# Kernel optimization log

Hardware: AMD Instinct MI355X
Metric: run time of the kernel (lower is better)

## Reference

```python
import jax, jax.numpy as jnp
import numpy as np

NUM_EMBEDDINGS = 1024
EMBEDDING_DIM = 64
COMMITMENT_COST = 0.25


def setup_inputs() -> dict:
    key = jax.random.key(0)
    k1, k2 = jax.random.split(key)
    inputs = jax.random.normal(k1, (64, 32, 32, EMBEDDING_DIM), dtype=jnp.float32)
    # matches nn.Embedding weight init: uniform(-1/K, 1/K)
    codebook = jax.random.uniform(
        k2, (NUM_EMBEDDINGS, EMBEDDING_DIM), dtype=jnp.float32,
        minval=-1.0 / NUM_EMBEDDINGS, maxval=1.0 / NUM_EMBEDDINGS)
    return {"inputs": inputs, "codebook": codebook}


def reference(inputs, codebook):
    input_shape = inputs.shape
    flat = inputs.reshape(-1, EMBEDDING_DIM)  # [N, D]
    distances = (jnp.sum(flat * flat, axis=1, keepdims=True)
                 + jnp.sum(codebook * codebook, axis=1)
                 - 2.0 * jnp.matmul(flat, codebook.T))
    encoding_indices = jnp.argmin(distances, axis=1)  # [N]
    quantized = codebook[encoding_indices].reshape(input_shape)
    codebook_loss = jnp.mean((jax.lax.stop_gradient(quantized) - inputs) ** 2)
    commitment_loss = jnp.mean((jax.lax.stop_gradient(inputs) - quantized) ** 2)
    vq_loss = codebook_loss + COMMITMENT_COST * commitment_loss
    # straight-through estimator
    quantized_st = inputs + jax.lax.stop_gradient(quantized - inputs)
    return quantized_st, vq_loss
```

## Files before the change

### kernel.cpp

```cpp
#include <hip/hip_runtime.h>

typedef __attribute__((ext_vector_type(8))) short short8;
typedef __attribute__((ext_vector_type(4))) float f32x4;
typedef __attribute__((ext_vector_type(4))) unsigned short u16x4;

#define NVEC 65536
#define DDIM 64
#define KCODES 1024
#define NELEM 4194304
#define CHUNK_C 128
#define VPB 128

__device__ inline unsigned short f2bf(float f) {
  unsigned u = __builtin_bit_cast(unsigned, f);
  return (unsigned short)((u + 0x7FFFu + ((u >> 16) & 1u)) >> 16);
}
__device__ inline float bf2f(unsigned short b) {
  unsigned u = ((unsigned)b) << 16;
  return __builtin_bit_cast(float, u);
}

__global__ __launch_bounds__(256) void vq_prep(const float* __restrict__ cb,
                                               unsigned short* __restrict__ cb_bf,
                                               float* __restrict__ en,
                                               float* __restrict__ out) {
  __shared__ float en_l[64];
  const int tid = threadIdx.x;
  if (tid < 64) en_l[tid] = 0.f;
  __syncthreads();
  const int base = blockIdx.x * 1024;
#pragma unroll
  for (int i = 0; i < 4; ++i) {
    int f = base + i * 256 + tid;
    float4 v = ((const float4*)cb)[f];
    unsigned short b0 = f2bf(v.x), b1 = f2bf(v.y), b2 = f2bf(v.z), b3 = f2bf(v.w);
    u16x4 pk = {b0, b1, b2, b3};
    *(u16x4*)(cb_bf + (size_t)f * 4) = pk;
    float e0 = bf2f(b0), e1 = bf2f(b1), e2 = bf2f(b2), e3 = bf2f(b3);
    atomicAdd(&en_l[(f >> 4) - blockIdx.x * 64], e0 * e0 + e1 * e1 + e2 * e2 + e3 * e3);
  }
  __syncthreads();
  if (tid < 64) en[blockIdx.x * 64 + tid] = en_l[tid];
  if (blockIdx.x == 0 && tid == 0) out[NELEM] = 0.f;
}

__global__ __launch_bounds__(256, 2) void vq_main(
    const float* __restrict__ x, const float* __restrict__ cb,
    const unsigned short* __restrict__ cb_bf, const float* __restrict__ en,
    float* __restrict__ out) {
  __shared__ alignas(16) unsigned short xs[8192];
  __shared__ alignas(16) unsigned short es[8192];
  __shared__ float en_s[CHUNK_C];
  __shared__ float xn[VPB];
  __shared__ float sbest[VPB];
  __shared__ int sidx[VPB];
  __shared__ float wsum[4];

  const int tid = threadIdx.x;
  const int wid = tid >> 6;
  const int L = tid & 63;
  const int q = L >> 4;
  const int c16 = L & 15;
  const int vblk = blockIdx.x * VPB;

  if (tid < VPB) xn[tid] = 0.f;
  __syncthreads();

#pragma unroll
  for (int i = 0; i < 4; ++i) {
    int f = i * 256 + tid;
    int fl = f & 63, fh = (f >> 6) & 1, fm = (f >> 7) & 1, fw = f >> 8;
    int v = fw * 32 + fm * 16 + (fl & 15);
    int d = fh * 32 + (fl >> 4) * 8;
    const float4* xp = (const float4*)(x + (size_t)(vblk + v) * DDIM + d);
    float4 u0 = xp[0], u1 = xp[1];
    unsigned short b0 = f2bf(u0.x), b1 = f2bf(u0.y), b2 = f2bf(u0.z), b3 = f2bf(u0.w);
    unsigned short b4 = f2bf(u1.x), b5 = f2bf(u1.y), b6 = f2bf(u1.z), b7 = f2bf(u1.w);
    float s0 = bf2f(b0), s1 = bf2f(b1), s2 = bf2f(b2), s3 = bf2f(b3);
    float s4 = bf2f(b4), s5 = bf2f(b5), s6 = bf2f(b6), s7 = bf2f(b7);
    atomicAdd(&xn[v], (s0 * s0 + s1 * s1 + s2 * s2 + s3 * s3) +
                          (s4 * s4 + s5 * s5 + s6 * s6 + s7 * s7));
    u16x4 p0 = {b0, b1, b2, b3}, p1 = {b4, b5, b6, b7};
    *(u16x4*)(xs + (size_t)f * 8) = p0;
    *(u16x4*)(xs + (size_t)f * 8 + 4) = p1;
  }
  __syncthreads();

  short8 a[2][2];
#pragma unroll
  for (int m = 0; m < 2; ++m)
#pragma unroll
    for (int h = 0; h < 2; ++h)
      a[m][h] = *(const short8*)(xs + (((wid * 4 + m * 2 + h) * 64 + L) * 8));

  float best[2][4];
  int bidx[2][4];
#pragma unroll
  for (int m = 0; m < 2; ++m)
#pragma unroll
    for (int r = 0; r < 4; ++r) {
      best[m][r] = 3.0e38f;
      bidx[m][r] = 0;
    }

  for (int c0 = 0; c0 < KCODES; c0 += CHUNK_C) {
    __syncthreads();
#pragma unroll
    for (int i = 0; i < 4; ++i) {
      int f = i * 256 + tid;
      int fl = f & 63, fh = (f >> 6) & 1, fnt = f >> 7;
      int code = c0 + fnt * 16 + (fl & 15);
      int d = fh * 32 + (fl >> 4) * 8;
      short8 v = *(const short8*)(cb_bf + (size_t)code * DDIM + d);
      *(short8*)(es + (size_t)f * 8) = v;
    }
    if (tid < CHUNK_C) en_s[tid] = en[c0 + tid];
    __syncthreads();

#pragma unroll
    for (int nt = 0; nt < 8; ++nt) {
      short8 b0 = *(const short8*)(es + ((nt * 2 + 0) * 64 + L) * 8);
      short8 b1 = *(const short8*)(es + ((nt * 2 + 1) * 64 + L) * 8);
      float env = en_s[nt * 16 + c16];
      int kidx = c0 + nt * 16 + c16;
#pragma unroll
      for (int m = 0; m < 2; ++m) {
        f32x4 z = {0.f, 0.f, 0.f, 0.f};
        f32x4 acc = __builtin_amdgcn_mfma_f32_16x16x32_bf16(a[m][0], b0, z, 0, 0, 0);
        acc = __builtin_amdgcn_mfma_f32_16x16x32_bf16(a[m][1], b1, acc, 0, 0, 0);
#pragma unroll
        for (int r = 0; r < 4; ++r) {
          float s = fmaf(-2.f, acc[r], env);
          if (s < best[m][r]) {
            best[m][r] = s;
            bidx[m][r] = kidx;
          }
        }
      }
    }
  }

#pragma unroll
  for (int m = 0; m < 2; ++m)
#pragma unroll
    for (int r = 0; r < 4; ++r) {
      float s = best[m][r];
      int id = bidx[m][r];
#pragma unroll
      for (int off = 1; off < 16; off <<= 1) {
        float s2 = __shfl_xor(s, off, 64);
        int i2 = __shfl_xor(id, off, 64);
        if (s2 < s || (s2 == s && i2 < id)) {
          s = s2;
          id = i2;
        }
      }
      if (c16 == 0) {
        int v = wid * 32 + m * 16 + q * 4 + r;
        sbest[v] = s;
        sidx[v] = id;
      }
    }
  __syncthreads();

#pragma unroll
  for (int i = 0; i < 8; ++i) {
    int f = i * 256 + tid;
    int v = f >> 4, d4 = f & 15;
    int id = sidx[v];
    float4 ev = ((const float4*)cb)[(size_t)id * 16 + d4];
    ((float4*)out)[(size_t)vblk * 16 + f] = ev;
  }

  float p = (tid < VPB) ? (sbest[tid] + xn[tid]) : 0.f;
#pragma unroll
  for (int off = 32; off >= 1; off >>= 1) p += __shfl_down(p, off, 64);
  if (L == 0) wsum[wid] = p;
  __syncthreads();
  if (tid == 0)
    atomicAdd(out + NELEM,
              ((wsum[0] + wsum[1]) + (wsum[2] + wsum[3])) * (1.25f / (float)NELEM));
}

extern "C" void kernel_launch(void* const* d_in, const int* in_sizes, int n_in,
                              void* d_out, int out_size, void* d_ws,
                              size_t ws_size, hipStream_t stream) {
  const float* x = (const float*)d_in[0];
  const float* cb = (const float*)d_in[1];
  float* out = (float*)d_out;
  char* ws = (char*)d_ws;
  unsigned short* cb_bf = (unsigned short*)ws;
  float* en = (float*)(ws + 131072);

  vq_prep<<<16, 256, 0, stream>>>(cb, cb_bf, en, out);
  vq_main<<<NVEC / VPB, 256, 0, stream>>>(x, cb, cb_bf, en, out);
}
```

Measured before the change: 102.3 us.

## Split codebook across waves, load operands directly, pack score and index keys

Each wave now covers 64 vectors by 512 codes. Input fragments are loaded straight from global into registers, and codebook fragments are read directly from global/L2 with no LDS staging or per-chunk barriers. The score and the index are packed into one unsigned key: the codebook norm is offset by 1.0 so the score stays positive, the low 10 mantissa bits are replaced by the index, and argmin becomes an integer min with a shared atomicMin across waves. This removes the LDS copies, the syncs and the compare/select pairs. In exchange it truncates score precision, which can change tie-breaking and slightly alter the loss, and it adds global-load latency in the inner loop.

```diff
diff --git a/kernel.cpp b/kernel.cpp
--- a/kernel.cpp
+++ b/kernel.cpp
@@ -8,158 +8,125 @@
 #define DDIM 64
 #define KCODES 1024
 #define NELEM 4194304
-#define CHUNK_C 128
 #define VPB 128
 
-__device__ inline unsigned short f2bf(float f) {
+static __device__ inline unsigned short f2bf(float f) {
   unsigned u = __builtin_bit_cast(unsigned, f);
   return (unsigned short)((u + 0x7FFFu + ((u >> 16) & 1u)) >> 16);
 }
-__device__ inline float bf2f(unsigned short b) {
-  unsigned u = ((unsigned)b) << 16;
-  return __builtin_bit_cast(float, u);
+static __device__ inline float bf2f(unsigned short b) {
+  return __builtin_bit_cast(float, (unsigned)b << 16);
 }
 
 __global__ __launch_bounds__(256) void vq_prep(const float* __restrict__ cb,
                                                unsigned short* __restrict__ cb_bf,
-                                               float* __restrict__ en,
+                                               float* __restrict__ en1,
                                                float* __restrict__ out) {
-  __shared__ float en_l[64];
-  const int tid = threadIdx.x;
-  if (tid < 64) en_l[tid] = 0.f;
-  __syncthreads();
-  const int base = blockIdx.x * 1024;
-#pragma unroll
-  for (int i = 0; i < 4; ++i) {
-    int f = base + i * 256 + tid;
-    float4 v = ((const float4*)cb)[f];
-    unsigned short b0 = f2bf(v.x), b1 = f2bf(v.y), b2 = f2bf(v.z), b3 = f2bf(v.w);
-    u16x4 pk = {b0, b1, b2, b3};
-    *(u16x4*)(cb_bf + (size_t)f * 4) = pk;
-    float e0 = bf2f(b0), e1 = bf2f(b1), e2 = bf2f(b2), e3 = bf2f(b3);
-    atomicAdd(&en_l[(f >> 4) - blockIdx.x * 64], e0 * e0 + e1 * e1 + e2 * e2 + e3 * e3);
-  }
-  __syncthreads();
-  if (tid < 64) en[blockIdx.x * 64 + tid] = en_l[tid];
-  if (blockIdx.x == 0 && tid == 0) out[NELEM] = 0.f;
+  int t = blockIdx.x * 256 + threadIdx.x;
+  float4 v = ((const float4*)cb)[t];
+  unsigned short b0 = f2bf(v.x), b1 = f2bf(v.y), b2 = f2bf(v.z), b3 = f2bf(v.w);
+  u16x4 pk = {b0, b1, b2, b3};
+  *(u16x4*)(cb_bf + (size_t)t * 4) = pk;
+  float e0 = bf2f(b0), e1 = bf2f(b1), e2 = bf2f(b2), e3 = bf2f(b3);
+  float s = (e0 * e0 + e1 * e1) + (e2 * e2 + e3 * e3);
+  s += __shfl_xor(s, 1, 64);
+  s += __shfl_xor(s, 2, 64);
+  s += __shfl_xor(s, 4, 64);
+  s += __shfl_xor(s, 8, 64);
+  if ((t & 15) == 0) en1[t >> 4] = 1.0f + s;
+  if (t == 0) out[NELEM] = 0.f;
 }
 
 __global__ __launch_bounds__(256, 2) void vq_main(
     const float* __restrict__ x, const float* __restrict__ cb,
-    const unsigned short* __restrict__ cb_bf, const float* __restrict__ en,
+    const unsigned short* __restrict__ cb_bf, const float* __restrict__ en1,
     float* __restrict__ out) {
-  __shared__ alignas(16) unsigned short xs[8192];
-  __shared__ alignas(16) unsigned short es[8192];
-  __shared__ float en_s[CHUNK_C];
+  __shared__ float en_s[KCODES];
+  __shared__ unsigned skey[VPB];
   __shared__ float xn[VPB];
-  __shared__ float sbest[VPB];
-  __shared__ int sidx[VPB];
   __shared__ float wsum[4];
 
   const int tid = threadIdx.x;
   const int wid = tid >> 6;
   const int L = tid & 63;
+  const int c16 = L & 15;
   const int q = L >> 4;
-  const int c16 = L & 15;
   const int vblk = blockIdx.x * VPB;
+  const int mbase = (wid & 1) * 64;
+  const int cbase = (wid >> 1) * 512;
 
-  if (tid < VPB) xn[tid] = 0.f;
-  __syncthreads();
+  ((float4*)en_s)[tid] = ((const float4*)en1)[tid];
+  if (tid < VPB) skey[tid] = 0xFFFFFFFFu;
 
+  short8 a[4][2];
 #pragma unroll
-  for (int i = 0; i < 4; ++i) {
-    int f = i * 256 + tid;
-    int fl = f & 63, fh = (f >> 6) & 1, fm = (f >> 7) & 1, fw = f >> 8;
-    int v = fw * 32 + fm * 16 + (fl & 15);
-    int d = fh * 32 + (fl >> 4) * 8;
-    const float4* xp = (const float4*)(x + (size_t)(vblk + v) * DDIM + d);
-    float4 u0 = xp[0], u1 = xp[1];
-    unsigned short b0 = f2bf(u0.x), b1 = f2bf(u0.y), b2 = f2bf(u0.z), b3 = f2bf(u0.w);
-    unsigned short b4 = f2bf(u1.x), b5 = f2bf(u1.y), b6 = f2bf(u1.z), b7 = f2bf(u1.w);
-    float s0 = bf2f(b0), s1 = bf2f(b1), s2 = bf2f(b2), s3 = bf2f(b3);
-    float s4 = bf2f(b4), s5 = bf2f(b5), s6 = bf2f(b6), s7 = bf2f(b7);
-    atomicAdd(&xn[v], (s0 * s0 + s1 * s1 + s2 * s2 + s3 * s3) +
-                          (s4 * s4 + s5 * s5 + s6 * s6 + s7 * s7));
-    u16x4 p0 = {b0, b1, b2, b3}, p1 = {b4, b5, b6, b7};
-    *(u16x4*)(xs + (size_t)f * 8) = p0;
-    *(u16x4*)(xs + (size_t)f * 8 + 4) = p1;
+  for (int mt = 0; mt < 4; ++mt) {
+    const float* xv = x + (size_t)(vblk + mbase + mt * 16 + c16) * DDIM + q * 8;
+    float4 u0 = *(const float4*)(xv);
+    float4 u1 = *(const float4*)(xv + 4);
+    float4 u2 = *(const float4*)(xv + 32);
+    float4 u3 = *(const float4*)(xv + 36);
+    unsigned short h0 = f2bf(u0.x), h1 = f2bf(u0.y), h2 = f2bf(u0.z), h3 = f2bf(u0.w);
+    unsigned short h4 = f2bf(u1.x), h5 = f2bf(u1.y), h6 = f2bf(u1.z), h7 = f2bf(u1.w);
+    unsigned short g0 = f2bf(u2.x), g1 = f2bf(u2.y), g2 = f2bf(u2.z), g3 = f2bf(u2.w);
+    unsigned short g4 = f2bf(u3.x), g5 = f2bf(u3.y), g6 = f2bf(u3.z), g7 = f2bf(u3.w);
+    short8 A0 = {(short)h0, (short)h1, (short)h2, (short)h3,
+                 (short)h4, (short)h5, (short)h6, (short)h7};
+    short8 A1 = {(short)g0, (short)g1, (short)g2, (short)g3,
+                 (short)g4, (short)g5, (short)g6, (short)g7};
+    a[mt][0] = A0;
+    a[mt][1] = A1;
+    float s0 = bf2f(h0), s1 = bf2f(h1), s2 = bf2f(h2), s3 = bf2f(h3);
+    float s4 = bf2f(h4), s5 = bf2f(h5), s6 = bf2f(h6), s7 = bf2f(h7);
+    float t0 = bf2f(g0), t1 = bf2f(g1), t2 = bf2f(g2), t3 = bf2f(g3);
+    float t4 = bf2f(g4), t5 = bf2f(g5), t6 = bf2f(g6), t7 = bf2f(g7);
+    float xs = ((s0 * s0 + s1 * s1) + (s2 * s2 + s3 * s3)) +
+               ((s4 * s4 + s5 * s5) + (s6 * s6 + s7 * s7)) +
+               ((t0 * t0 + t1 * t1) + (t2 * t2 + t3 * t3)) +
+               ((t4 * t4 + t5 * t5) + (t6 * t6 + t7 * t7));
+    xs += __shfl_xor(xs, 16, 64);
+    xs += __shfl_xor(xs, 32, 64);
+    if (wid < 2 && L < 16) xn[mbase + mt * 16 + L] = xs;
   }
   __syncthreads();
 
-  short8 a[2][2];
+  unsigned bestk[4][4];
 #pragma unroll
-  for (int m = 0; m < 2; ++m)
+  for (int m = 0; m < 4; ++m)
 #pragma unroll
-    for (int h = 0; h < 2; ++h)
-      a[m][h] = *(const short8*)(xs + (((wid * 4 + m * 2 + h) * 64 + L) * 8));
+    for (int r = 0; r < 4; ++r) bestk[m][r] = 0xFFFFFFFFu;
 
-  float best[2][4];
-  int bidx[2][4];
+  const unsigned short* bptr = cb_bf + (size_t)(cbase + c16) * DDIM + q * 8;
+#pragma unroll 2
+  for (int nt = 0; nt < 32; ++nt) {
+    short8 b0 = *(const short8*)(bptr + nt * 16 * DDIM);
+    short8 b1 = *(const short8*)(bptr + nt * 16 * DDIM + 32);
+    float env = en_s[cbase + nt * 16 + c16];
+    unsigned kidx = (unsigned)(cbase + nt * 16 + c16);
 #pragma unroll
-  for (int m = 0; m < 2; ++m)
+    for (int m = 0; m < 4; ++m) {
+      f32x4 z = {0.f, 0.f, 0.f, 0.f};
+      f32x4 acc = __builtin_amdgcn_mfma_f32_16x16x32_bf16(a[m][0], b0, z, 0, 0, 0);
+      acc = __builtin_amdgcn_mfma_f32_16x16x32_bf16(a[m][1], b1, acc, 0, 0, 0);
 #pragma unroll
-    for (int r = 0; r < 4; ++r) {
-      best[m][r] = 3.0e38f;
-      bidx[m][r] = 0;
-    }
-
-  for (int c0 = 0; c0 < KCODES; c0 += CHUNK_C) {
-    __syncthreads();
-#pragma unroll
-    for (int i = 0; i < 4; ++i) {
-      int f = i * 256 + tid;
-      int fl = f & 63, fh = (f >> 6) & 1, fnt = f >> 7;
-      int code = c0 + fnt * 16 + (fl & 15);
-      int d = fh * 32 + (fl >> 4) * 8;
-      short8 v = *(const short8*)(cb_bf + (size_t)code * DDIM + d);
-      *(short8*)(es + (size_t)f * 8) = v;
-    }
-    if (tid < CHUNK_C) en_s[tid] = en[c0 + tid];
-    __syncthreads();
-
-#pragma unroll
-    for (int nt = 0; nt < 8; ++nt) {
-      short8 b0 = *(const short8*)(es + ((nt * 2 + 0) * 64 + L) * 8);
-      short8 b1 = *(const short8*)(es + ((nt * 2 + 1) * 64 + L) * 8);
-      float env = en_s[nt * 16 + c16];
-      int kidx = c0 + nt * 16 + c16;
-#pragma unroll
-      for (int m = 0; m < 2; ++m) {
-        f32x4 z = {0.f, 0.f, 0.f, 0.f};
-        f32x4 acc = __builtin_amdgcn_mfma_f32_16x16x32_bf16(a[m][0], b0, z, 0, 0, 0);
-        acc = __builtin_amdgcn_mfma_f32_16x16x32_bf16(a[m][1], b1, acc, 0, 0, 0);
-#pragma unroll
-        for (int r = 0; r < 4; ++r) {
-          float s = fmaf(-2.f, acc[r], env);
-          if (s < best[m][r]) {
-            best[m][r] = s;
-            bidx[m][r] = kidx;
-          }
-        }
+      for (int r = 0; r < 4; ++r) {
+        float p = fmaf(-2.f, acc[r], env);
+        unsigned key = (__builtin_bit_cast(unsigned, p) & 0xFFFFFC00u) | kidx;
+        bestk[m][r] = key < bestk[m][r] ? key : bestk[m][r];
       }
     }
   }
 
 #pragma unroll
-  for (int m = 0; m < 2; ++m)
+  for (int m = 0; m < 4; ++m)
 #pragma unroll
     for (int r = 0; r < 4; ++r) {
-      float s = best[m][r];
-      int id = bidx[m][r];
-#pragma unroll
-      for (int off = 1; off < 16; off <<= 1) {
-        float s2 = __shfl_xor(s, off, 64);
-        int i2 = __shfl_xor(id, off, 64);
-        if (s2 < s || (s2 == s && i2 < id)) {
-          s = s2;
-          id = i2;
-        }
-      }
-      if (c16 == 0) {
-        int v = wid * 32 + m * 16 + q * 4 + r;
-        sbest[v] = s;
-        sidx[v] = id;
-      }
+      unsigned k = bestk[m][r];
+      k = min(k, (unsigned)__shfl_xor((int)k, 1, 64));
+      k = min(k, (unsigned)__shfl_xor((int)k, 2, 64));
+      k = min(k, (unsigned)__shfl_xor((int)k, 4, 64));
+      k = min(k, (unsigned)__shfl_xor((int)k, 8, 64));
+      if (c16 == 0) atomicMin(&skey[mbase + m * 16 + q * 4 + r], k);
     }
   __syncthreads();
 
@@ -167,15 +134,19 @@
   for (int i = 0; i < 8; ++i) {
     int f = i * 256 + tid;
     int v = f >> 4, d4 = f & 15;
-    int id = sidx[v];
-    float4 ev = ((const float4*)cb)[(size_t)id * 16 + d4];
-    ((float4*)out)[(size_t)vblk * 16 + f] = ev;
+    int id = (int)(skey[v] & 1023u);
+    ((float4*)out)[(size_t)vblk * 16 + f] = ((const float4*)cb)[(size_t)id * 16 + d4];
   }
 
-  float p = (tid < VPB) ? (sbest[tid] + xn[tid]) : 0.f;
+  float pl = 0.f;
+  if (tid < VPB) {
+    unsigned k = skey[tid];
+    float pt = __builtin_bit_cast(float, k & 0xFFFFFC00u);
+    pl = (pt - 1.0f) + xn[tid];
+  }
 #pragma unroll
-  for (int off = 32; off >= 1; off >>= 1) p += __shfl_down(p, off, 64);
-  if (L == 0) wsum[wid] = p;
+  for (int off = 32; off >= 1; off >>= 1) pl += __shfl_down(pl, off, 64);
+  if (L == 0) wsum[wid] = pl;
   __syncthreads();
   if (tid == 0)
     atomicAdd(out + NELEM,
@@ -190,8 +161,8 @@
   float* out = (float*)d_out;
   char* ws = (char*)d_ws;
   unsigned short* cb_bf = (unsigned short*)ws;
-  float* en = (float*)(ws + 131072);
+  float* en1 = (float*)(ws + 131072);
 
-  vq_prep<<<16, 256, 0, stream>>>(cb, cb_bf, en, out);
-  vq_main<<<NVEC / VPB, 256, 0, stream>>>(x, cb, cb_bf, en, out);
+  vq_prep<<<64, 256, 0, stream>>>(cb, cb_bf, en1, out);
+  vq_main<<<NVEC / VPB, 256, 0, stream>>>(x, cb, cb_bf, en1, out);
 }
```

New measurement: 97.34 us. 4.8% less time.
